# Performance work log

Hardware: AMD Instinct MI355X
Metric: run time of the kernel (lower is better)

Reference implementation:

```python
import jax, jax.numpy as jnp
import numpy as np

B, CIN, H, W = 16, 256, 48, 48
K, CD, MULTI = 64, 64, 1
GAMMA = (1.0 - 1e-10) ** (1.0 ** 0.6)  # iter = 1


def _ln(v, s, b, eps=1e-5):
    m = v.mean(-1, keepdims=True)
    var = ((v - m) ** 2).mean(-1, keepdims=True)
    return (v - m) / jnp.sqrt(var + eps) * s + b


def _spatial_masks():
    # pairwise squared distance between (i,j) grid coords, N = H*W
    ii, jj = jnp.meshgrid(jnp.arange(H, dtype=jnp.float32), jnp.arange(W, dtype=jnp.float32), indexing='ij')
    coord = jnp.stack([ii.ravel(), jj.ravel()], axis=1)  # [N,2]
    sq = (coord ** 2).sum(-1, keepdims=True)             # [N,1]
    d2 = sq - 2.0 * (coord @ coord.T) + sq.T             # [N,N]
    m = jnp.exp(-jnp.sqrt(jnp.abs(d2)))
    A = m / m.sum(0, keepdims=True)  # column-normalized (torch sums dim=1 of [B,N,N])
    cur, out = A, []
    for _ in range(MULTI):
        cur = cur @ A  # A^(num+2)
        out.append(cur)
    return out


def setup_inputs() -> dict:
    key = jax.random.key(0)
    ks = jax.random.split(key, 3)
    x = jax.random.normal(ks[0], (B, CIN, H, W), jnp.float32)
    clusters = jax.random.normal(ks[1], (1, K, CD), jnp.float32) * 0.1
    pi = jnp.ones((1, K), jnp.float32) / K
    cov = jnp.ones((1, K), jnp.float32)
    w_proj = jax.random.normal(ks[2], (CD, CIN), jnp.float32) / np.sqrt(CIN)
    nt_scale = jnp.ones((CD,), jnp.float32)
    nt_bias = jnp.zeros((CD,), jnp.float32)
    pn_scale = jnp.ones((K * MULTI,), jnp.float32)
    pn_bias = jnp.zeros((K * MULTI,), jnp.float32)
    return dict(x=x, clusters=clusters, pi=pi, cov=cov, w_proj=w_proj,
                nt_scale=nt_scale, nt_bias=nt_bias, pn_scale=pn_scale, pn_bias=pn_bias)


def reference(x, clusters, pi, cov, w_proj, nt_scale, nt_bias, pn_scale, pn_bias):
    N = H * W
    # 1x1 conv projection -> tokens [B,N,CD]
    xf = jnp.einsum('bihw,ci->bhwc', x, w_proj).reshape(B, N, CD)
    # normalized templates (batch-invariant)
    t = _ln(clusters[0], nt_scale, nt_bias)  # [K,CD]
    # squared euclidean distance via expansion (avoids [B,CD,N,K] intermediate)
    x2 = (xf ** 2).sum(-1)  # [B,N]
    t2 = (t ** 2).sum(-1)   # [K]
    d = x2[:, :, None] + t2[None, None, :] - 2.0 * jnp.einsum('bnc,kc->bnk', xf, t)
    logits = jnp.log(pi[0] / jnp.sqrt(cov[0])) - d / cov[0] / 2.0
    attn = jax.nn.softmax(logits, axis=-1)  # [B,N,K]
    # EM-style updates
    pi_new = pi + GAMMA * (attn.sum(1) / N - pi)                     # [B,K]
    attn_n = attn + 1e-8
    attn_n = attn_n / attn_n.sum(-2, keepdims=True)                  # normalize over N
    t_new = clusters + GAMMA * (jnp.einsum('bnc,bnk->bkc', xf, attn_n) - clusters)  # [B,K,CD]
    tn2 = (t_new ** 2).sum(-1)  # [B,K]
    d2 = x2[:, :, None] + tn2[:, None, :] - 2.0 * jnp.einsum('bnc,bkc->bnk', xf, t_new)
    cov_new = cov + GAMMA * ((d2 * attn_n).sum(1) - cov)             # [B,K]
    # spatial distance-encoding masks (stop-gradient / constant w.r.t. params)
    masks = _spatial_masks()
    outp = jnp.concatenate([jnp.einsum('bnk,nm->bkm', attn_n, M) for M in masks], axis=1)  # [B,K*MULTI,N]
    outp = _ln(outp.transpose(0, 2, 1), pn_scale, pn_bias).transpose(0, 2, 1)
    outp = outp.reshape(B, K * MULTI, H, W)
    attn_out = attn.transpose(0, 2, 1).reshape(B, K, H, W)
    return outp, attn_out, t_new, pi_new, cov_new
```

## Files before the change

kernel.cpp:

```cpp
#include <hip/hip_runtime.h>
#include <hip/hip_bf16.h>
#include <math.h>

#define B_   16
#define CIN_ 256
#define H_   48
#define W_   48
#define N_   2304
#define K_   64
#define CD_  64

#define GAMMA_F 0.9999999999f
#define KSPLIT 1152

using f32x4  = __attribute__((ext_vector_type(4))) float;
using bf16x8 = __attribute__((ext_vector_type(8))) short;
using s16x4  = __attribute__((ext_vector_type(4))) short;

__device__ __forceinline__ void split_bf(float x, short& hi, short& lo) {
  unsigned u = __builtin_bit_cast(unsigned, x);
  unsigned r = (u + 0x7FFFu + ((u >> 16) & 1u)) & 0xFFFF0000u;
  hi = (short)(r >> 16);
  float res = x - __builtin_bit_cast(float, r);
  unsigned u2 = __builtin_bit_cast(unsigned, res);
  unsigned r2 = u2 + 0x7FFFu + ((u2 >> 16) & 1u);
  lo = (short)(r2 >> 16);
}

constexpr size_t OFF_XF    = 0;
constexpr size_t OFF_ANT   = OFF_XF    + (size_t)B_*N_*CD_;
constexpr size_t OFF_T     = OFF_ANT   + (size_t)B_*K_*N_;
constexpr size_t OFF_T2    = OFF_T     + (size_t)K_*CD_;
constexpr size_t OFF_LOGPI = OFF_T2    + K_;
constexpr size_t OFF_I2C   = OFF_LOGPI + K_;
constexpr size_t OFF_X2    = OFF_I2C   + K_;
constexpr size_t OFF_CS    = OFF_X2    + (size_t)B_*N_;
constexpr size_t OFF_ICN   = OFF_CS    + (size_t)B_*K_;
constexpr size_t OFF_MASKH = OFF_ICN   + (size_t)B_*K_;
constexpr size_t OFF_MASKL = OFF_MASKH + (size_t)N_*N_/2;

constexpr size_t OUT_OUTP = 0;
constexpr size_t OUT_ATTN = (size_t)B_*K_*N_;
constexpr size_t OUT_TNEW = OUT_ATTN + (size_t)B_*K_*N_;
constexpr size_t OUT_PI   = OUT_TNEW + (size_t)B_*K_*CD_;
constexpr size_t OUT_COV  = OUT_PI   + (size_t)B_*K_;

__global__ __launch_bounds__(256) void k_proj(const float* __restrict__ x, const float* __restrict__ wp,
                                              float* __restrict__ xf) {
  __shared__ float xs[32][64];
  __shared__ float ws_[32][65];
  int b = blockIdx.y, n0 = blockIdx.x * 64;
  int tid = threadIdx.x;
  int nn = tid & 63, cg = tid >> 6;
  float acc[16];
#pragma unroll
  for (int j = 0; j < 16; j++) acc[j] = 0.f;
  for (int i0 = 0; i0 < CIN_; i0 += 32) {
#pragma unroll
    for (int j = 0; j < 8; j++) {
      int ii = cg * 8 + j;
      xs[ii][nn] = x[((size_t)b * CIN_ + i0 + ii) * N_ + n0 + nn];
    }
    {
      int c = tid >> 2, iq = (tid & 3) * 8;
#pragma unroll
      for (int j = 0; j < 8; j++)
        ws_[iq + j][c] = wp[(size_t)c * CIN_ + i0 + iq + j];
    }
    __syncthreads();
#pragma unroll
    for (int ii = 0; ii < 32; ++ii) {
      float xv = xs[ii][nn];
#pragma unroll
      for (int j = 0; j < 16; j++) acc[j] += xv * ws_[ii][cg * 16 + j];
    }
    __syncthreads();
  }
  float* dst = xf + ((size_t)b * N_ + n0 + nn) * CD_ + cg * 16;
#pragma unroll
  for (int j4 = 0; j4 < 4; j4++)
    *(float4*)(dst + j4 * 4) = make_float4(acc[j4*4], acc[j4*4+1], acc[j4*4+2], acc[j4*4+3]);
}

__global__ void k_templ(const float* __restrict__ clusters, const float* __restrict__ pi,
                        const float* __restrict__ cov, const float* __restrict__ nsc,
                        const float* __restrict__ nbi, float* __restrict__ t, float* __restrict__ t2,
                        float* __restrict__ logpi, float* __restrict__ i2c) {
  int k = threadIdx.x;
  float v[CD_];
  float m = 0;
#pragma unroll
  for (int c = 0; c < CD_; c++) { v[c] = clusters[k * CD_ + c]; m += v[c]; }
  m /= CD_;
  float var = 0;
#pragma unroll
  for (int c = 0; c < CD_; c++) { float d = v[c] - m; var += d * d; }
  var /= CD_;
  float inv = 1.f / sqrtf(var + 1e-5f);
  float s2 = 0;
#pragma unroll
  for (int c = 0; c < CD_; c++) {
    float tv = (v[c] - m) * inv * nsc[c] + nbi[c];
    t[k * CD_ + c] = tv;
    s2 += tv * tv;
  }
  t2[k] = s2;
  float p = pi[k], cv = cov[k];
  logpi[k] = logf(p) - 0.5f * logf(cv);
  i2c[k] = 0.5f / cv;
}

__global__ __launch_bounds__(256) void k_attn(const float* __restrict__ xf, const float* __restrict__ t,
                                              const float* __restrict__ t2, const float* __restrict__ logpi,
                                              const float* __restrict__ i2c,
                                              float* __restrict__ aout, float* __restrict__ x2o) {
  __shared__ __align__(16) float ts[K_][72];
  __shared__ float t2s[K_], lps[K_], ics[K_];
  int tid = threadIdx.x;
  for (int i = tid; i < K_ * CD_; i += 256) ts[i >> 6][i & 63] = t[i];
  if (tid < K_) { t2s[tid] = t2[tid]; lps[tid] = logpi[tid]; ics[tid] = i2c[tid]; }
  __syncthreads();
  int b = blockIdx.y;
  int tok = tid >> 2, kg = tid & 3;
  int n = blockIdx.x * 64 + tok;
  const float4* xr = (const float4*)(xf + ((size_t)b * N_ + n) * CD_);
  float4 xv[16];
#pragma unroll
  for (int i = 0; i < 16; i++) xv[i] = xr[i];
  float x2 = 0;
#pragma unroll
  for (int i = 0; i < 16; i++) x2 += xv[i].x * xv[i].x + xv[i].y * xv[i].y + xv[i].z * xv[i].z + xv[i].w * xv[i].w;
  if (kg == 0) x2o[(size_t)b * N_ + n] = x2;
  float lg[16];
#pragma unroll
  for (int kk = 0; kk < 16; kk++) {
    int k = kk * 4 + kg;
    const float4* tk = (const float4*)&ts[k][0];
    float d0 = 0, d1 = 0, d2 = 0, d3 = 0;
#pragma unroll
    for (int i = 0; i < 16; i += 4) {
      float4 t0 = tk[i], t1 = tk[i + 1], t2v = tk[i + 2], t3 = tk[i + 3];
      d0 += xv[i].x * t0.x + xv[i].y * t0.y + xv[i].z * t0.z + xv[i].w * t0.w;
      d1 += xv[i+1].x * t1.x + xv[i+1].y * t1.y + xv[i+1].z * t1.z + xv[i+1].w * t1.w;
      d2 += xv[i+2].x * t2v.x + xv[i+2].y * t2v.y + xv[i+2].z * t2v.z + xv[i+2].w * t2v.w;
      d3 += xv[i+3].x * t3.x + xv[i+3].y * t3.y + xv[i+3].z * t3.z + xv[i+3].w * t3.w;
    }
    float dot = (d0 + d1) + (d2 + d3);
    lg[kk] = lps[k] - (x2 + t2s[k] - 2.f * dot) * ics[k];
  }
  float mx = lg[0];
#pragma unroll
  for (int kk = 1; kk < 16; kk++) mx = fmaxf(mx, lg[kk]);
  mx = fmaxf(mx, __shfl_xor(mx, 1));
  mx = fmaxf(mx, __shfl_xor(mx, 2));
  float sum = 0;
#pragma unroll
  for (int kk = 0; kk < 16; kk++) { lg[kk] = __expf(lg[kk] - mx); sum += lg[kk]; }
  sum += __shfl_xor(sum, 1);
  sum += __shfl_xor(sum, 2);
  float inv = 1.f / sum;
  size_t base = (size_t)b * K_ * N_ + n;
#pragma unroll
  for (int kk = 0; kk < 16; kk++)
    aout[base + (size_t)(kk * 4 + kg) * N_] = lg[kk] * inv;
}

__global__ __launch_bounds__(256) void k_colsum2(const float* __restrict__ ant, float* __restrict__ colsum) {
  int r = blockIdx.x, tid = threadIdx.x;
  const float* row = ant + (size_t)r * N_;
  float s = 0;
  for (int n = tid; n < N_; n += 256) s += row[n];
#pragma unroll
  for (int off = 32; off; off >>= 1) s += __shfl_down(s, off);
  __shared__ float red[4];
  if ((tid & 63) == 0) red[tid >> 6] = s;
  __syncthreads();
  if (tid == 0) colsum[r] = red[0] + red[1] + red[2] + red[3];
}

__global__ void k_pinew(const float* __restrict__ colsum, const float* __restrict__ pi,
                        float* __restrict__ pi_out, float* __restrict__ icn) {
  int b = blockIdx.x, k = threadIdx.x;
  float cs = colsum[b * K_ + k];
  float p = pi[k];
  pi_out[b * K_ + k] = p + GAMMA_F * (cs / (float)N_ - p);
  icn[b * K_ + k] = 1.f / (cs + (float)N_ * 1e-8f);
}

__global__ __launch_bounds__(256) void k_tnew_cov(const float* __restrict__ ant, const float* __restrict__ icn,
                                                  const float* __restrict__ xf, const float* __restrict__ x2,
                                                  const float* __restrict__ clusters, const float* __restrict__ cov,
                                                  float* __restrict__ tnew_out, float* __restrict__ cov_out) {
  int k = blockIdx.x, b = blockIdx.y;
  int tid = threadIdx.x;
  int c = tid & 63, g = tid >> 6;
  const float* arow = ant + ((size_t)b * K_ + k) * N_;
  const float* x2r = x2 + (size_t)b * N_;
  float acc = 0, ax2 = 0;
#pragma unroll 4
  for (int n = g; n < N_; n += 4) {
    float a = arow[n] + 1e-8f;
    acc += a * xf[((size_t)b * N_ + n) * CD_ + c];
    ax2 += a * x2r[n];
  }
  __shared__ float red[4][64];
  __shared__ float red2[4];
  red[g][c] = acc;
  if (c == 0) red2[g] = ax2;
  __syncthreads();
  if (tid < 64) {
    float icnv = icn[b * K_ + k];
    float s = (red[0][c] + red[1][c] + red[2][c] + red[3][c]) * icnv;
    float cl = clusters[k * CD_ + c];
    float tv = cl + GAMMA_F * (s - cl);
    tnew_out[((size_t)b * K_ + k) * CD_ + c] = tv;
    float sq = tv * tv;
    float st = s * tv;
#pragma unroll
    for (int off = 32; off; off >>= 1) { sq += __shfl_down(sq, off); st += __shfl_down(st, off); }
    if (c == 0) {
      float ax2t = (red2[0] + red2[1] + red2[2] + red2[3]) * icnv;
      float cv = cov[k];
      float csum = ax2t + sq - 2.f * st;
      cov_out[b * K_ + k] = cv + GAMMA_F * (csum - cv);
    }
  }
}

__global__ __launch_bounds__(256) void k_acenter(const float* __restrict__ attn, const float* __restrict__ icn,
                                                 short* __restrict__ AcH, short* __restrict__ AcL) {
  int b = blockIdx.y;
  int n = blockIdx.x * 256 + threadIdx.x;
  const float* base = attn + (size_t)b * K_ * N_ + n;
  const float* ic = icn + b * K_;
  float a[K_];
  float s = 0;
#pragma unroll 8
  for (int k = 0; k < K_; k++) {
    a[k] = base[(size_t)k * N_];
    s += (a[k] + 1e-8f) * ic[k];
  }
  float amean = s * (1.f / (float)K_);
#pragma unroll 8
  for (int k = 0; k < K_; k++) {
    float icv = ic[k];
    float va = fmaf(a[k], icv, 1e-8f * icv) - amean;
    short h, l;
    split_bf(va, h, l);
    AcH[(size_t)(b * K_ + k) * N_ + n] = h;
    AcL[(size_t)(b * K_ + k) * N_ + n] = l;
  }
}

__global__ __launch_bounds__(256) void k_mask(short* __restrict__ MH, short* __restrict__ ML) {
  __shared__ float red[4];
  const int m = blockIdx.x;
  const int mi = m / W_, mj = m % W_;
  const int tid = threadIdx.x;
  float e[N_ / 256];
  float s = 0;
#pragma unroll
  for (int it = 0; it < N_ / 256; it++) {
    int n = it * 256 + tid;
    int ni = n / W_, nj = n - (n / W_) * W_;
    int dx = ni - mi, dy = nj - mj;
    e[it] = __expf(-sqrtf((float)(dx * dx + dy * dy)));
    s += e[it];
  }
#pragma unroll
  for (int off = 32; off; off >>= 1) s += __shfl_down(s, off);
  if ((tid & 63) == 0) red[tid >> 6] = s;
  __syncthreads();
  const float imc = 1.f / (red[0] + red[1] + red[2] + red[3]);
#pragma unroll
  for (int it = 0; it < N_ / 256; it++) {
    int n = it * 256 + tid;
    short h, l;
    split_bf(e[it] * imc, h, l);
    MH[(size_t)m * N_ + n] = h;
    ML[(size_t)m * N_ + n] = l;
  }
}


template<int GEMM>
__global__ __launch_bounds__(256) void gemm_splitk(const short* __restrict__ AH, const short* __restrict__ AL,
                                                   const short* __restrict__ MaskH, const short* __restrict__ MaskL,
                                                   float* __restrict__ P0, float* __restrict__ P1) {
  __shared__ __align__(16) short Ah[2][64][40];
  __shared__ __align__(16) short Al[2][64][40];
  __shared__ __align__(16) short Bh[2][64][40];
  __shared__ __align__(16) short Bl[2][64][40];
  const int tid = threadIdx.x;
  const int b = blockIdx.y;
  const int z = blockIdx.z;
  const int m0 = b * 64, n0 = blockIdx.x * 64;
  const int lane = tid & 63, w = tid >> 6;
  const int fr = lane & 15, quad = lane >> 4;
  const int wr = (w >> 1) * 32;
  const int wc = (w & 1) * 32;
  const int srow = tid >> 2;
  const int skq  = (tid & 3) * 8;
  const int zb = z * KSPLIT;
  const size_t mrow = (size_t)(n0 + srow) * N_;
  const size_t abase = (size_t)(m0 + srow) * N_ + skq;
  f32x4 acc[2][2] = {};
  bf16x8 ah = *(const bf16x8*)&AH[abase + zb];
  bf16x8 al = *(const bf16x8*)&AL[abase + zb];
  bf16x8 mh = *(const bf16x8*)&MaskH[mrow + zb + skq];
  bf16x8 ml = *(const bf16x8*)&MaskL[mrow + zb + skq];
  for (int it = 0; it < KSPLIT / 32; ++it) {
    const int c = it & 1;
    *(bf16x8*)&Ah[c][srow][skq] = ah;
    *(bf16x8*)&Al[c][srow][skq] = al;
    *(bf16x8*)&Bh[c][srow][skq] = mh;
    *(bf16x8*)&Bl[c][srow][skq] = ml;
    if (it + 1 < KSPLIT / 32) {
      const int kn = zb + (it + 1) * 32;
      ah = *(const bf16x8*)&AH[abase + kn];
      al = *(const bf16x8*)&AL[abase + kn];
      mh = *(const bf16x8*)&MaskH[mrow + kn + skq];
      ml = *(const bf16x8*)&MaskL[mrow + kn + skq];
    }
    __syncthreads();
    bf16x8 afh[2], afl[2], bfh[2], bfl[2];
#pragma unroll
    for (int i = 0; i < 2; i++) {
      afh[i] = *(const bf16x8*)&Ah[c][wr + i * 16 + fr][quad * 8];
      afl[i] = *(const bf16x8*)&Al[c][wr + i * 16 + fr][quad * 8];
      bfh[i] = *(const bf16x8*)&Bh[c][wc + i * 16 + fr][quad * 8];
      bfl[i] = *(const bf16x8*)&Bl[c][wc + i * 16 + fr][quad * 8];
    }
#pragma unroll
    for (int i = 0; i < 2; i++)
#pragma unroll
      for (int j = 0; j < 2; j++) {
        acc[i][j] = __builtin_amdgcn_mfma_f32_16x16x32_bf16(afh[i], bfh[j], acc[i][j], 0, 0, 0);
        acc[i][j] = __builtin_amdgcn_mfma_f32_16x16x32_bf16(afh[i], bfl[j], acc[i][j], 0, 0, 0);
        acc[i][j] = __builtin_amdgcn_mfma_f32_16x16x32_bf16(afl[i], bfh[j], acc[i][j], 0, 0, 0);
      }
  }
  float* P = z ? P1 : P0;
#pragma unroll
  for (int i = 0; i < 2; i++)
#pragma unroll
    for (int j = 0; j < 2; j++)
      *(f32x4*)&P[(size_t)(m0 + wr + i * 16 + fr) * N_ + n0 + wc + j * 16 + quad * 4] = acc[i][j];
}

__global__ __launch_bounds__(256) void k_combine1(const float* __restrict__ P0, const float* __restrict__ P1,
                                                  short* __restrict__ YdH, short* __restrict__ YdL) {
  const int b = blockIdx.y, n0 = blockIdx.x * 64;
  const int tid = threadIdx.x;
  const int row = tid >> 2, coff = (tid & 3) * 16;
  const size_t base = (size_t)(b * 64 + row) * N_ + n0 + coff;
#pragma unroll
  for (int q = 0; q < 4; q++) {
    float4 a = *(const float4*)&P0[base + q * 4];
    float4 d = *(const float4*)&P1[base + q * 4];
    s16x4 h4, l4;
    short h, l;
    split_bf(a.x + d.x, h, l); h4[0] = h; l4[0] = l;
    split_bf(a.y + d.y, h, l); h4[1] = h; l4[1] = l;
    split_bf(a.z + d.z, h, l); h4[2] = h; l4[2] = l;
    split_bf(a.w + d.w, h, l); h4[3] = h; l4[3] = l;
    *(s16x4*)&YdH[base + q * 4] = h4;
    *(s16x4*)&YdL[base + q * 4] = l4;
  }
}

__global__ __launch_bounds__(256) void k_combine2_ln(const float* __restrict__ Q0, const float* __restrict__ Q1,
                                                     const float* __restrict__ pns, const float* __restrict__ pnb,
                                                     float* __restrict__ outp) {
  __shared__ __align__(16) float S[64][68];
  __shared__ float rstd[64], sc[64], bi[64];
  const int b = blockIdx.y, n0 = blockIdx.x * 64;
  const int tid = threadIdx.x;
  const int m0 = b * 64;
  if (tid < 64) { sc[tid] = pns[tid]; bi[tid] = pnb[tid]; }
  const int row = tid >> 2, coff = (tid & 3) * 16;
  const size_t base = (size_t)(m0 + row) * N_ + n0 + coff;
#pragma unroll
  for (int q = 0; q < 4; q++) {
    float4 a = *(const float4*)&Q0[base + q * 4];
    float4 d = *(const float4*)&Q1[base + q * 4];
    *(f32x4*)&S[row][coff + q * 4] = f32x4{a.x + d.x, a.y + d.y, a.z + d.z, a.w + d.w};
  }
  __syncthreads();
  if (tid < 64) {
    float ss = 0;
#pragma unroll
    for (int k = 0; k < K_; k++) { float d = S[k][tid]; ss += d * d; }
    rstd[tid] = 1.f / sqrtf(ss / (float)K_ + 1e-5f);
  }
  __syncthreads();
  {
    int c = tid & 63, g = tid >> 6;
#pragma unroll
    for (int i = 0; i < 16; i++) {
      int r = g * 16 + i;
      outp[(size_t)(m0 + r) * N_ + n0 + c] = S[r][c] * rstd[c] * sc[r] + bi[r];
    }
  }
}

extern "C" void kernel_launch(void* const* d_in, const int* in_sizes, int n_in,
                              void* d_out, int out_size, void* d_ws, size_t ws_size,
                              hipStream_t stream) {
  const float* x        = (const float*)d_in[0];
  const float* clusters = (const float*)d_in[1];
  const float* pi       = (const float*)d_in[2];
  const float* cov      = (const float*)d_in[3];
  const float* w_proj   = (const float*)d_in[4];
  const float* nt_scale = (const float*)d_in[5];
  const float* nt_bias  = (const float*)d_in[6];
  const float* pn_scale = (const float*)d_in[7];
  const float* pn_bias  = (const float*)d_in[8];
  float* out = (float*)d_out;
  float* w = (float*)d_ws;
  short* AcH = (short*)(w + OFF_ANT);
  short* AcL = AcH + (size_t)B_ * K_ * N_;
  short* YdH = AcH;
  short* YdL = AcL;
  short* MaskH = (short*)(w + OFF_MASKH);
  short* MaskL = (short*)(w + OFF_MASKL);
  float* attn = out + OUT_ATTN;
  float* Phalf0 = w + OFF_XF;
  float* Phalf1 = out + OUT_OUTP;

  k_mask<<<N_, 256, 0, stream>>>(MaskH, MaskL);
  k_proj<<<dim3(N_ / 64, B_), 256, 0, stream>>>(x, w_proj, w + OFF_XF);
  k_templ<<<1, K_, 0, stream>>>(clusters, pi, cov, nt_scale, nt_bias,
                                w + OFF_T, w + OFF_T2, w + OFF_LOGPI, w + OFF_I2C);
  k_attn<<<dim3(N_ / 64, B_), 256, 0, stream>>>(w + OFF_XF, w + OFF_T, w + OFF_T2,
                                                w + OFF_LOGPI, w + OFF_I2C,
                                                attn, w + OFF_X2);
  k_colsum2<<<B_ * K_, 256, 0, stream>>>(attn, w + OFF_CS);
  k_pinew<<<B_, K_, 0, stream>>>(w + OFF_CS, pi, out + OUT_PI, w + OFF_ICN);
  k_acenter<<<dim3(N_ / 256, B_), 256, 0, stream>>>(attn, w + OFF_ICN, AcH, AcL);
  k_tnew_cov<<<dim3(K_, B_), 256, 0, stream>>>(attn, w + OFF_ICN, w + OFF_XF, w + OFF_X2,
                                               clusters, cov, out + OUT_TNEW, out + OUT_COV);
  gemm_splitk<1><<<dim3(N_ / 64, B_, 2), 256, 0, stream>>>(AcH, AcL, MaskH, MaskL, Phalf0, Phalf1);
  k_combine1<<<dim3(N_ / 64, B_), 256, 0, stream>>>(Phalf0, Phalf1, YdH, YdL);
  gemm_splitk<2><<<dim3(N_ / 64, B_, 2), 256, 0, stream>>>(YdH, YdL, MaskH, MaskL, Phalf0, Phalf1);
  k_combine2_ln<<<dim3(N_ / 64, B_), 256, 0, stream>>>(Phalf0, Phalf1, pn_scale, pn_bias, out + OUT_OUTP);
}
```

Baseline: 361.9 us.

## Use direct global-to-LDS loads with XOR-swizzled shared tiles in split-K mask GEMM

The split-K mask GEMM now stages its A and mask tiles with global_load_lds, which writes straight into shared memory instead of going through registers. The padded shared arrays are replaced by unpadded ones whose 8-element chunks are XOR-swizzled by row, so fragment reads avoid bank conflicts. The loop is restructured so the next tile is issued into the other buffer before compute, with one barrier at the end of each iteration. This is meant to cut register pressure and load-issue overhead and to overlap memory with MFMA work. It relies on the compiler inserting the right vmcnt waits before the barrier, and on the swizzle matching between writer and reader.

```diff
diff --git a/kernel.cpp b/kernel.cpp
--- a/kernel.cpp
+++ b/kernel.cpp
@@ -25,6 +25,12 @@
   unsigned u2 = __builtin_bit_cast(unsigned, res);
   unsigned r2 = u2 + 0x7FFFu + ((u2 >> 16) & 1u);
   lo = (short)(r2 >> 16);
+}
+
+__device__ __forceinline__ void gload16(const short* g, short* l) {
+  __builtin_amdgcn_global_load_lds(
+      (const __attribute__((address_space(1))) unsigned int*)g,
+      (__attribute__((address_space(3))) unsigned int*)l, 16, 0, 0);
 }
 
 constexpr size_t OFF_XF    = 0;
@@ -287,10 +293,10 @@
 __global__ __launch_bounds__(256) void gemm_splitk(const short* __restrict__ AH, const short* __restrict__ AL,
                                                    const short* __restrict__ MaskH, const short* __restrict__ MaskL,
                                                    float* __restrict__ P0, float* __restrict__ P1) {
-  __shared__ __align__(16) short Ah[2][64][40];
-  __shared__ __align__(16) short Al[2][64][40];
-  __shared__ __align__(16) short Bh[2][64][40];
-  __shared__ __align__(16) short Bl[2][64][40];
+  __shared__ __align__(16) short Ah[2][64][32];
+  __shared__ __align__(16) short Al[2][64][32];
+  __shared__ __align__(16) short Bh[2][64][32];
+  __shared__ __align__(16) short Bl[2][64][32];
   const int tid = threadIdx.x;
   const int b = blockIdx.y;
   const int z = blockIdx.z;
@@ -300,36 +306,37 @@
   const int wr = (w >> 1) * 32;
   const int wc = (w & 1) * 32;
   const int srow = tid >> 2;
-  const int skq  = (tid & 3) * 8;
+  const int sq   = (tid & 3) ^ ((tid >> 3) & 3);
+  const int skq  = sq * 8;
   const int zb = z * KSPLIT;
-  const size_t mrow = (size_t)(n0 + srow) * N_;
   const size_t abase = (size_t)(m0 + srow) * N_ + skq;
+  const size_t mbase = (size_t)(n0 + srow) * N_ + skq;
+  short* ldsA_h = &Ah[0][0][0] + tid * 8;
+  short* ldsA_l = &Al[0][0][0] + tid * 8;
+  short* ldsB_h = &Bh[0][0][0] + tid * 8;
+  short* ldsB_l = &Bl[0][0][0] + tid * 8;
+  auto stage = [&](int c, int kk) {
+    gload16(&AH[abase + kk], ldsA_h + c * 2048);
+    gload16(&AL[abase + kk], ldsA_l + c * 2048);
+    gload16(&MaskH[mbase + kk], ldsB_h + c * 2048);
+    gload16(&MaskL[mbase + kk], ldsB_l + c * 2048);
+  };
+  const int rsw = (fr >> 1) & 3;
+  const int rq  = (quad ^ rsw) * 8;
   f32x4 acc[2][2] = {};
-  bf16x8 ah = *(const bf16x8*)&AH[abase + zb];
-  bf16x8 al = *(const bf16x8*)&AL[abase + zb];
-  bf16x8 mh = *(const bf16x8*)&MaskH[mrow + zb + skq];
-  bf16x8 ml = *(const bf16x8*)&MaskL[mrow + zb + skq];
-  for (int it = 0; it < KSPLIT / 32; ++it) {
+  stage(0, zb);
+  __syncthreads();
+  constexpr int NT = KSPLIT / 32;
+  for (int it = 0; it < NT; ++it) {
     const int c = it & 1;
-    *(bf16x8*)&Ah[c][srow][skq] = ah;
-    *(bf16x8*)&Al[c][srow][skq] = al;
-    *(bf16x8*)&Bh[c][srow][skq] = mh;
-    *(bf16x8*)&Bl[c][srow][skq] = ml;
-    if (it + 1 < KSPLIT / 32) {
-      const int kn = zb + (it + 1) * 32;
-      ah = *(const bf16x8*)&AH[abase + kn];
-      al = *(const bf16x8*)&AL[abase + kn];
-      mh = *(const bf16x8*)&MaskH[mrow + kn + skq];
-      ml = *(const bf16x8*)&MaskL[mrow + kn + skq];
-    }
-    __syncthreads();
+    if (it + 1 < NT) stage(c ^ 1, zb + (it + 1) * 32);
     bf16x8 afh[2], afl[2], bfh[2], bfl[2];
 #pragma unroll
     for (int i = 0; i < 2; i++) {
-      afh[i] = *(const bf16x8*)&Ah[c][wr + i * 16 + fr][quad * 8];
-      afl[i] = *(const bf16x8*)&Al[c][wr + i * 16 + fr][quad * 8];
-      bfh[i] = *(const bf16x8*)&Bh[c][wc + i * 16 + fr][quad * 8];
-      bfl[i] = *(const bf16x8*)&Bl[c][wc + i * 16 + fr][quad * 8];
+      afh[i] = *(const bf16x8*)&Ah[c][wr + i * 16 + fr][rq];
+      afl[i] = *(const bf16x8*)&Al[c][wr + i * 16 + fr][rq];
+      bfh[i] = *(const bf16x8*)&Bh[c][wc + i * 16 + fr][rq];
+      bfl[i] = *(const bf16x8*)&Bl[c][wc + i * 16 + fr][rq];
     }
 #pragma unroll
     for (int i = 0; i < 2; i++)
@@ -339,6 +346,7 @@
         acc[i][j] = __builtin_amdgcn_mfma_f32_16x16x32_bf16(afh[i], bfl[j], acc[i][j], 0, 0, 0);
         acc[i][j] = __builtin_amdgcn_mfma_f32_16x16x32_bf16(afl[i], bfh[j], acc[i][j], 0, 0, 0);
       }
+    __syncthreads();
   }
   float* P = z ? P1 : P0;
 #pragma unroll
```

After: 374.5 us. 1.03x slower.

## Store bf16 split operands in MFMA fragment layout and load fragments directly

Applied to the files above, without the earlier changes.

The producers of the split-bf16 GEMM operands (attention-centered, mask and combine1 kernels) now write in a tiled 16-row by 8-k fragment layout. The split-K GEMM then loads MFMA fragments straight from global memory into registers, with register double-buffering, and drops the LDS staging and __syncthreads. This removes LDS traffic and barriers from the GEMM. In exchange, operands shared between waves are no longer reused through LDS, and the producer kernels do scattered 2-byte stores.

```diff
diff --git a/kernel.cpp b/kernel.cpp
--- a/kernel.cpp
+++ b/kernel.cpp
@@ -25,6 +25,10 @@
   unsigned u2 = __builtin_bit_cast(unsigned, res);
   unsigned r2 = u2 + 0x7FFFu + ((u2 >> 16) & 1u);
   lo = (short)(r2 >> 16);
+}
+
+__device__ __forceinline__ size_t fm(int row, int k) {
+  return (size_t)(row >> 4) * (16 * N_) + (size_t)(k >> 3) * 128 + (row & 15) * 8 + (k & 7);
 }
 
 constexpr size_t OFF_XF    = 0;
@@ -241,14 +245,16 @@
     s += (a[k] + 1e-8f) * ic[k];
   }
   float amean = s * (1.f / (float)K_);
+  const size_t noff = (size_t)(n >> 3) * 128 + (n & 7);
 #pragma unroll 8
   for (int k = 0; k < K_; k++) {
     float icv = ic[k];
     float va = fmaf(a[k], icv, 1e-8f * icv) - amean;
     short h, l;
     split_bf(va, h, l);
-    AcH[(size_t)(b * K_ + k) * N_ + n] = h;
-    AcL[(size_t)(b * K_ + k) * N_ + n] = l;
+    size_t dst = (size_t)(b * 4 + (k >> 4)) * (16 * N_) + (k & 15) * 8 + noff;
+    AcH[dst] = h;
+    AcL[dst] = l;
   }
 }
 
@@ -272,13 +278,15 @@
   if ((tid & 63) == 0) red[tid >> 6] = s;
   __syncthreads();
   const float imc = 1.f / (red[0] + red[1] + red[2] + red[3]);
+  const size_t rowpart = (size_t)(m >> 4) * (16 * N_) + (m & 15) * 8;
 #pragma unroll
   for (int it = 0; it < N_ / 256; it++) {
     int n = it * 256 + tid;
     short h, l;
     split_bf(e[it] * imc, h, l);
-    MH[(size_t)m * N_ + n] = h;
-    ML[(size_t)m * N_ + n] = l;
+    size_t dst = rowpart + (size_t)(n >> 3) * 128 + (n & 7);
+    MH[dst] = h;
+    ML[dst] = l;
   }
 }
 
@@ -287,10 +295,6 @@
 __global__ __launch_bounds__(256) void gemm_splitk(const short* __restrict__ AH, const short* __restrict__ AL,
                                                    const short* __restrict__ MaskH, const short* __restrict__ MaskL,
                                                    float* __restrict__ P0, float* __restrict__ P1) {
-  __shared__ __align__(16) short Ah[2][64][40];
-  __shared__ __align__(16) short Al[2][64][40];
-  __shared__ __align__(16) short Bh[2][64][40];
-  __shared__ __align__(16) short Bl[2][64][40];
   const int tid = threadIdx.x;
   const int b = blockIdx.y;
   const int z = blockIdx.z;
@@ -299,46 +303,42 @@
   const int fr = lane & 15, quad = lane >> 4;
   const int wr = (w >> 1) * 32;
   const int wc = (w & 1) * 32;
-  const int srow = tid >> 2;
-  const int skq  = (tid & 3) * 8;
   const int zb = z * KSPLIT;
-  const size_t mrow = (size_t)(n0 + srow) * N_;
-  const size_t abase = (size_t)(m0 + srow) * N_ + skq;
+  size_t aoff[2], boff[2];
+#pragma unroll
+  for (int i = 0; i < 2; i++) {
+    aoff[i] = (size_t)((m0 + wr + i * 16) >> 4) * (16 * N_) + quad * 128 + fr * 8;
+    boff[i] = (size_t)((n0 + wc + i * 16) >> 4) * (16 * N_) + quad * 128 + fr * 8;
+  }
   f32x4 acc[2][2] = {};
-  bf16x8 ah = *(const bf16x8*)&AH[abase + zb];
-  bf16x8 al = *(const bf16x8*)&AL[abase + zb];
-  bf16x8 mh = *(const bf16x8*)&MaskH[mrow + zb + skq];
-  bf16x8 ml = *(const bf16x8*)&MaskL[mrow + zb + skq];
-  for (int it = 0; it < KSPLIT / 32; ++it) {
-    const int c = it & 1;
-    *(bf16x8*)&Ah[c][srow][skq] = ah;
-    *(bf16x8*)&Al[c][srow][skq] = al;
-    *(bf16x8*)&Bh[c][srow][skq] = mh;
-    *(bf16x8*)&Bl[c][srow][skq] = ml;
-    if (it + 1 < KSPLIT / 32) {
-      const int kn = zb + (it + 1) * 32;
-      ah = *(const bf16x8*)&AH[abase + kn];
-      al = *(const bf16x8*)&AL[abase + kn];
-      mh = *(const bf16x8*)&MaskH[mrow + kn + skq];
-      ml = *(const bf16x8*)&MaskL[mrow + kn + skq];
-    }
-    __syncthreads();
-    bf16x8 afh[2], afl[2], bfh[2], bfl[2];
+  bf16x8 ah[2], al[2], bh[2], bl[2];
+#pragma unroll
+  for (int i = 0; i < 2; i++) {
+    ah[i] = *(const bf16x8*)&AH[aoff[i] + (size_t)zb * 16];
+    al[i] = *(const bf16x8*)&AL[aoff[i] + (size_t)zb * 16];
+    bh[i] = *(const bf16x8*)&MaskH[boff[i] + (size_t)zb * 16];
+    bl[i] = *(const bf16x8*)&MaskL[boff[i] + (size_t)zb * 16];
+  }
+  for (int k0 = zb; k0 < zb + KSPLIT; k0 += 32) {
+    const size_t kn = (size_t)((k0 + 32 < zb + KSPLIT) ? k0 + 32 : k0) * 16;
+    bf16x8 ah1[2], al1[2], bh1[2], bl1[2];
 #pragma unroll
     for (int i = 0; i < 2; i++) {
-      afh[i] = *(const bf16x8*)&Ah[c][wr + i * 16 + fr][quad * 8];
-      afl[i] = *(const bf16x8*)&Al[c][wr + i * 16 + fr][quad * 8];
-      bfh[i] = *(const bf16x8*)&Bh[c][wc + i * 16 + fr][quad * 8];
-      bfl[i] = *(const bf16x8*)&Bl[c][wc + i * 16 + fr][quad * 8];
+      ah1[i] = *(const bf16x8*)&AH[aoff[i] + kn];
+      al1[i] = *(const bf16x8*)&AL[aoff[i] + kn];
+      bh1[i] = *(const bf16x8*)&MaskH[boff[i] + kn];
+      bl1[i] = *(const bf16x8*)&MaskL[boff[i] + kn];
     }
 #pragma unroll
     for (int i = 0; i < 2; i++)
 #pragma unroll
       for (int j = 0; j < 2; j++) {
-        acc[i][j] = __builtin_amdgcn_mfma_f32_16x16x32_bf16(afh[i], bfh[j], acc[i][j], 0, 0, 0);
-        acc[i][j] = __builtin_amdgcn_mfma_f32_16x16x32_bf16(afh[i], bfl[j], acc[i][j], 0, 0, 0);
-        acc[i][j] = __builtin_amdgcn_mfma_f32_16x16x32_bf16(afl[i], bfh[j], acc[i][j], 0, 0, 0);
+        acc[i][j] = __builtin_amdgcn_mfma_f32_16x16x32_bf16(ah[i], bh[j], acc[i][j], 0, 0, 0);
+        acc[i][j] = __builtin_amdgcn_mfma_f32_16x16x32_bf16(ah[i], bl[j], acc[i][j], 0, 0, 0);
+        acc[i][j] = __builtin_amdgcn_mfma_f32_16x16x32_bf16(al[i], bh[j], acc[i][j], 0, 0, 0);
       }
+#pragma unroll
+    for (int i = 0; i < 2; i++) { ah[i] = ah1[i]; al[i] = al1[i]; bh[i] = bh1[i]; bl[i] = bl1[i]; }
   }
   float* P = z ? P1 : P0;
 #pragma unroll
@@ -354,6 +354,7 @@
   const int tid = threadIdx.x;
   const int row = tid >> 2, coff = (tid & 3) * 16;
   const size_t base = (size_t)(b * 64 + row) * N_ + n0 + coff;
+  const size_t rowpart = (size_t)(b * 4 + (row >> 4)) * (16 * N_) + (row & 15) * 8;
 #pragma unroll
   for (int q = 0; q < 4; q++) {
     float4 a = *(const float4*)&P0[base + q * 4];
@@ -364,8 +365,10 @@
     split_bf(a.y + d.y, h, l); h4[1] = h; l4[1] = l;
     split_bf(a.z + d.z, h, l); h4[2] = h; l4[2] = l;
     split_bf(a.w + d.w, h, l); h4[3] = h; l4[3] = l;
-    *(s16x4*)&YdH[base + q * 4] = h4;
-    *(s16x4*)&YdL[base + q * 4] = l4;
+    const int col = n0 + coff + q * 4;
+    const size_t dst = rowpart + (size_t)(col >> 3) * 128 + (col & 7);
+    *(s16x4*)&YdH[dst] = h4;
+    *(s16x4*)&YdL[dst] = l4;
   }
 }
 
```

New measurement: 372.9 us. +3.0%, slower.
